# Performance work log

Hardware: AMD Instinct MI355X
Metric: run time of the kernel (lower is better)

## Reference

```python
import jax, jax.numpy as jnp
import numpy as np

B, T, TM, D, H, FF = 4, 1024, 1024, 1024, 16, 4096
HS = D // H
EPS = 1e-5


def _layer_norm(x, g, b):
    m = jnp.mean(x, axis=-1, keepdims=True)
    v = jnp.mean(jnp.square(x - m), axis=-1, keepdims=True)
    return (x - m) / jnp.sqrt(v + EPS) * g + b


def _mha(q_in, k_in, v_in, wq, bq, wk, bk, wv, bv, wo, bo):
    b, t, c = q_in.shape
    tm = k_in.shape[1]
    q = (q_in @ wq + bq).reshape(b, t, H, HS).transpose(0, 2, 1, 3)   # [b,h,t,hs]
    k = (k_in @ wk + bk).reshape(b, tm, H, HS).transpose(0, 2, 1, 3)  # [b,h,tm,hs]
    v = (v_in @ wv + bv).reshape(b, tm, H, HS).transpose(0, 2, 1, 3)
    att = jnp.einsum('bhtd,bhsd->bhts', q, k) * (1.0 / np.sqrt(HS))
    att = jax.nn.softmax(att, axis=-1)                                # [b,h,t,tm]
    y = jnp.einsum('bhts,bhsd->bhtd', att, v)
    y = y.transpose(0, 2, 1, 3).reshape(b, t, c)
    y = y @ wo + bo
    return y, att.mean(axis=1)                                        # attn avg over heads


def setup_inputs() -> dict:
    key = jax.random.key(0)
    ks = jax.random.split(key, 32)
    s = 0.02
    w = lambda k, shape: (jax.random.normal(k, shape, jnp.float32) * s)
    inp = {
        'tgt': jax.random.normal(ks[0], (B, T, D), jnp.float32),
        'memory': jax.random.normal(ks[1], (B, TM, D), jnp.float32),
        # self-attention params
        'sa_wq': w(ks[2], (D, D)), 'sa_bq': jnp.zeros((D,), jnp.float32),
        'sa_wk': w(ks[3], (D, D)), 'sa_bk': jnp.zeros((D,), jnp.float32),
        'sa_wv': w(ks[4], (D, D)), 'sa_bv': jnp.zeros((D,), jnp.float32),
        'sa_wo': w(ks[5], (D, D)), 'sa_bo': jnp.zeros((D,), jnp.float32),
        # cross-attention params
        'ca_wq': w(ks[6], (D, D)), 'ca_bq': jnp.zeros((D,), jnp.float32),
        'ca_wk': w(ks[7], (D, D)), 'ca_bk': jnp.zeros((D,), jnp.float32),
        'ca_wv': w(ks[8], (D, D)), 'ca_bv': jnp.zeros((D,), jnp.float32),
        'ca_wo': w(ks[9], (D, D)), 'ca_bo': jnp.zeros((D,), jnp.float32),
        # FFN
        'w1': w(ks[10], (D, FF)), 'b1': jnp.zeros((FF,), jnp.float32),
        'w2': w(ks[11], (FF, D)), 'b2': jnp.zeros((D,), jnp.float32),
        # LayerNorms
        'ln1_g': jnp.ones((D,), jnp.float32), 'ln1_b': jnp.zeros((D,), jnp.float32),
        'ln2_g': jnp.ones((D,), jnp.float32), 'ln2_b': jnp.zeros((D,), jnp.float32),
        'ln3_g': jnp.ones((D,), jnp.float32), 'ln3_b': jnp.zeros((D,), jnp.float32),
    }
    return inp


def reference(tgt, memory,
              sa_wq, sa_bq, sa_wk, sa_bk, sa_wv, sa_bv, sa_wo, sa_bo,
              ca_wq, ca_bq, ca_wk, ca_bk, ca_wv, ca_bv, ca_wo, ca_bo,
              w1, b1, w2, b2,
              ln1_g, ln1_b, ln2_g, ln2_b, ln3_g, ln3_b):
    x = tgt
    tmp, _ = _mha(x, x, x, sa_wq, sa_bq, sa_wk, sa_bk, sa_wv, sa_bv, sa_wo, sa_bo)
    x = _layer_norm(x + tmp, ln1_g, ln1_b)
    tmp, attention = _mha(x, memory, memory,
                          ca_wq, ca_bq, ca_wk, ca_bk, ca_wv, ca_bv, ca_wo, ca_bo)
    x = _layer_norm(x + tmp, ln2_g, ln2_b)
    tmp = jax.nn.relu(x @ w1 + b1) @ w2 + b2
    x = _layer_norm(x + tmp, ln3_g, ln3_b)
    return x, attention
```

## Files before the change

### kernel.cpp

```cpp
#include <hip/hip_runtime.h>
#include <hip/hip_bf16.h>
#include <cstdint>
#include <cstddef>

using u16 = unsigned short;
typedef __attribute__((ext_vector_type(4))) float f32x4;
typedef __attribute__((ext_vector_type(8))) short bf16x8;
typedef __attribute__((ext_vector_type(4))) short bf16x4;

constexpr int Bc = 4, Tc = 1024, TMc = 1024, Dc = 1024, Hc = 16, HSc = 64, FFc = 4096;
constexpr int BT = Bc * Tc;

__device__ __forceinline__ u16 f2bf(float f) {
  union { float f; uint32_t u; } v; v.f = f;
  uint32_t u = v.u;
  u += 0x7fffu + ((u >> 16) & 1u);
  return (u16)(u >> 16);
}

__device__ __forceinline__ bf16x8 cat8(bf16x4 lo, bf16x4 hi) {
  bf16x8 r;
  r[0] = lo[0]; r[1] = lo[1]; r[2] = lo[2]; r[3] = lo[3];
  r[4] = hi[0]; r[5] = hi[1]; r[6] = hi[2]; r[7] = hi[3];
  return r;
}

__device__ __forceinline__ void gload16(const u16* g, u16* l) {
  __builtin_amdgcn_global_load_lds((const __attribute__((address_space(1))) void*)g,
                                   (__attribute__((address_space(3))) void*)l, 16, 0, 0);
}

__global__ __launch_bounds__(256)
void tconv(const float* __restrict__ in, u16* __restrict__ outp, int K, int N)
{
  __shared__ u16 tile[64][65];
  const int tx = threadIdx.x & 15, ty = threadIdx.x >> 4;
  const int kb = blockIdx.y * 64, nb = blockIdx.x * 64;
  #pragma unroll
  for (int i = 0; i < 4; ++i) {
    const int r = ty + i * 16;
    const float4 v = *(const float4*)(in + (size_t)(kb + r) * N + nb + tx * 4);
    tile[r][tx * 4 + 0] = f2bf(v.x);
    tile[r][tx * 4 + 1] = f2bf(v.y);
    tile[r][tx * 4 + 2] = f2bf(v.z);
    tile[r][tx * 4 + 3] = f2bf(v.w);
  }
  __syncthreads();
  #pragma unroll
  for (int i = 0; i < 4; ++i) {
    const int n = ty + i * 16;
    bf16x4 o;
    o[0] = (short)tile[tx * 4 + 0][n];
    o[1] = (short)tile[tx * 4 + 1][n];
    o[2] = (short)tile[tx * 4 + 2][n];
    o[3] = (short)tile[tx * 4 + 3][n];
    *(bf16x4*)(outp + (size_t)(nb + n) * K + kb + tx * 4) = o;
  }
}

__global__ __launch_bounds__(256)
void cvt_bf16(const float* __restrict__ in, u16* __restrict__ outp, int n4)
{
  const int i = blockIdx.x * 256 + threadIdx.x;
  if (i < n4) {
    const float4 v = ((const float4*)in)[i];
    bf16x4 o;
    o[0] = (short)f2bf(v.x); o[1] = (short)f2bf(v.y);
    o[2] = (short)f2bf(v.z); o[3] = (short)f2bf(v.w);
    ((bf16x4*)outp)[i] = o;
  }
}

template<int MODE, int BMv, int DEPTH>
__global__ __launch_bounds__((BMv == 256) ? 512 : 256)
void gemm_bt(const u16* __restrict__ A, const u16* __restrict__ Bt,
             const float* __restrict__ bias, const float* __restrict__ resid,
             void* __restrict__ outp, int M, int N, int K)
{
  constexpr int BM = BMv, BN = 128, BK = 32;
  constexpr int NTHR = (BM == 256) ? 512 : 256;
  constexpr int RPC = NTHR / 4;
  constexpr int ACALLS = BM / RPC;
  constexpr int BCALLS = BN / RPC;
  constexpr int CALLS = ACALLS + BCALLS;
  constexpr int NB = DEPTH + 1;
  __shared__ __align__(16) u16 As[NB][BM * BK];
  __shared__ __align__(16) u16 Bs[NB][BN * BK];
  const int tid = threadIdx.x;
  const int lane = tid & 63, w = tid >> 6;
  const int wr = w >> 1, wc = w & 1;
  const int hi4 = lane >> 4, lr = lane & 15;

  const int nwg = gridDim.x;
  const int GX = N / BN;
  const int bid0 = (int)blockIdx.x;
  const int L = (bid0 & 7) * (nwg >> 3) + (bid0 >> 3);
  const int bandw = 8 * GX;
  const int band = L / bandw;
  const int rem = L - band * bandw;
  const int m0 = (band * 8 + (rem & 7)) * BM;
  const int n0 = (rem >> 3) * BN;

  const int srow = tid >> 2;
  const int gslot = (tid & 3) ^ ((srow >> 1) & 3);
  const u16* ga = A  + (size_t)(m0 + srow) * K + gslot * 8;
  const u16* gb = Bt + (size_t)(n0 + srow) * K + gslot * 8;
  const int wofs = w * 512;
  const int cswz = (lr >> 1) & 3;

  auto stage = [&](int buf, int kt) {
    #pragma unroll
    for (int j = 0; j < ACALLS; ++j)
      gload16(ga + (size_t)j * RPC * K + kt, &As[buf][j * NTHR * 8 + wofs]);
    #pragma unroll
    for (int j = 0; j < BCALLS; ++j)
      gload16(gb + (size_t)j * RPC * K + kt, &Bs[buf][j * NTHR * 8 + wofs]);
  };

  f32x4 acc[4][4] = {};
  const int nt = K / BK;

  #pragma unroll
  for (int p = 0; p < DEPTH; ++p)
    if (p < nt) stage(p % NB, p * BK);

  int cur = 0;
  for (int t = 0; t < nt; ++t) {
    {
      const int ahead = nt - 1 - t;
      const int cap = (ahead < DEPTH - 1 ? ahead : DEPTH - 1) * CALLS;
      switch (cap) {
        case 0:  asm volatile("s_waitcnt vmcnt(0)"  ::: "memory"); break;
        case 3:  asm volatile("s_waitcnt vmcnt(3)"  ::: "memory"); break;
        case 4:  asm volatile("s_waitcnt vmcnt(4)"  ::: "memory"); break;
        case 8:  asm volatile("s_waitcnt vmcnt(8)"  ::: "memory"); break;
        default: asm volatile("s_waitcnt vmcnt(12)" ::: "memory"); break;
      }
    }
    __builtin_amdgcn_s_barrier();
    __builtin_amdgcn_sched_barrier(0);

    if (t + DEPTH < nt) {
      int b2 = cur + DEPTH; if (b2 >= NB) b2 -= NB;
      stage(b2, (t + DEPTH) * BK);
    }

    bf16x8 af[4], bfr[4];
    #pragma unroll
    for (int mb = 0; mb < 4; ++mb)
      af[mb] = *(const bf16x8*)&As[cur][(wr * 64 + mb * 16 + lr) * BK + (hi4 ^ cswz) * 8];
    #pragma unroll
    for (int nb = 0; nb < 4; ++nb)
      bfr[nb] = *(const bf16x8*)&Bs[cur][(wc * 64 + nb * 16 + lr) * BK + (hi4 ^ cswz) * 8];
    #pragma unroll
    for (int mb = 0; mb < 4; ++mb)
      #pragma unroll
      for (int nb = 0; nb < 4; ++nb)
        acc[mb][nb] = __builtin_amdgcn_mfma_f32_16x16x32_bf16(af[mb], bfr[nb], acc[mb][nb], 0, 0, 0);

    ++cur; if (cur == NB) cur = 0;
  }

  const int orow = m0 + wr * 64 + 4 * hi4;
  const int ocol = n0 + wc * 64 + lr;
  #pragma unroll
  for (int nb = 0; nb < 4; ++nb) {
    const int c = ocol + nb * 16;
    const float bv = bias ? bias[c] : 0.0f;
    #pragma unroll
    for (int mb = 0; mb < 4; ++mb) {
      #pragma unroll
      for (int r = 0; r < 4; ++r) {
        const size_t idx = (size_t)(orow + mb * 16 + r) * N + c;
        float v = acc[mb][nb][r] + bv;
        if (MODE == 1) {
          ((float*)outp)[idx] = v + resid[idx];
        } else {
          if (MODE == 2) v = fmaxf(v, 0.0f);
          ((u16*)outp)[idx] = f2bf(v);
        }
      }
    }
  }
}

__global__ __launch_bounds__(256)
void flash_attn(const u16* __restrict__ Q, const u16* __restrict__ Kb,
                const u16* __restrict__ Vb, u16* __restrict__ Y,
                float* __restrict__ Mout, float* __restrict__ Lout,
                int qstr, int kstr)
{
  constexpr int LDK = 72;
  __shared__ __align__(16) u16 Ks[64 * LDK];
  __shared__ __align__(16) u16 Vt[64 * LDK];
  const int tid = threadIdx.x, lane = tid & 63, w = tid >> 6;
  const int hi4 = lane >> 4, lr = lane & 15;
  const int bh = blockIdx.y, b = bh >> 4, h = bh & 15;
  const int q0 = blockIdx.x * 64 + w * 16;

  bf16x8 qf[2];
  {
    const u16* qp = Q + ((size_t)(b * Tc + q0 + lr)) * qstr + h * HSc;
    #pragma unroll
    for (int ks = 0; ks < 2; ++ks)
      qf[ks] = cat8(*(const bf16x4*)(qp + ks * 32 + 4 * hi4),
                    *(const bf16x4*)(qp + ks * 32 + 16 + 4 * hi4));
  }

  float m_run = -1e30f, l_run = 0.0f;
  f32x4 o[4] = {};

  const int krow = tid >> 3, kcol = (tid & 7) * 8;
  const int vs = tid >> 4, vd = (tid & 15) * 4;

  for (int s0 = 0; s0 < TMc; s0 += 64) {
    const u16* kp = Kb + ((size_t)(b * TMc + s0 + krow)) * kstr + h * HSc + kcol;
    *(bf16x8*)&Ks[krow * LDK + kcol]        = *(const bf16x8*)kp;
    *(bf16x8*)&Ks[(krow + 32) * LDK + kcol] = *(const bf16x8*)(kp + (size_t)32 * kstr);
    #pragma unroll
    for (int rr = 0; rr < 4; ++rr) {
      const int ss = vs + rr * 16;
      bf16x4 vv = *(const bf16x4*)(Vb + ((size_t)(b * TMc + s0 + ss)) * kstr + h * HSc + vd);
      Vt[(vd + 0) * LDK + ss] = (u16)vv[0];
      Vt[(vd + 1) * LDK + ss] = (u16)vv[1];
      Vt[(vd + 2) * LDK + ss] = (u16)vv[2];
      Vt[(vd + 3) * LDK + ss] = (u16)vv[3];
    }
    __syncthreads();

    f32x4 st[4];
    #pragma unroll
    for (int kb2 = 0; kb2 < 4; ++kb2) {
      f32x4 a = {};
      #pragma unroll
      for (int ks = 0; ks < 2; ++ks) {
        const u16* p = &Ks[(kb2 * 16 + lr) * LDK + ks * 32 + 4 * hi4];
        bf16x8 kf = cat8(*(const bf16x4*)p, *(const bf16x4*)(p + 16));
        a = __builtin_amdgcn_mfma_f32_16x16x32_bf16(kf, qf[ks], a, 0, 0, 0);
      }
      st[kb2] = a;
    }

    float cmax = -1e30f;
    #pragma unroll
    for (int kb2 = 0; kb2 < 4; ++kb2)
      #pragma unroll
      for (int r = 0; r < 4; ++r) {
        st[kb2][r] *= 0.125f;
        cmax = fmaxf(cmax, st[kb2][r]);
      }
    cmax = fmaxf(cmax, __shfl_xor(cmax, 16));
    cmax = fmaxf(cmax, __shfl_xor(cmax, 32));
    const float m_new = fmaxf(m_run, cmax);
    const float sc = __expf(m_run - m_new);
    float psum = 0.0f;
    #pragma unroll
    for (int kb2 = 0; kb2 < 4; ++kb2)
      #pragma unroll
      for (int r = 0; r < 4; ++r) {
        const float e = __expf(st[kb2][r] - m_new);
        st[kb2][r] = e;
        psum += e;
      }
    psum += __shfl_xor(psum, 16);
    psum += __shfl_xor(psum, 32);
    l_run = l_run * sc + psum;
    m_run = m_new;

    #pragma unroll
    for (int r = 0; r < 4; ++r) {
      const float osc = __shfl(sc, 4 * hi4 + r);
      #pragma unroll
      for (int nb = 0; nb < 4; ++nb) o[nb][r] *= osc;
    }

    bf16x8 pa[2];
    #pragma unroll
    for (int ks = 0; ks < 2; ++ks) {
      bf16x8 t;
      #pragma unroll
      for (int i = 0; i < 4; ++i) t[i]     = (short)f2bf(st[2 * ks + 0][i]);
      #pragma unroll
      for (int i = 0; i < 4; ++i) t[4 + i] = (short)f2bf(st[2 * ks + 1][i]);
      pa[ks] = t;
    }
    #pragma unroll
    for (int nb = 0; nb < 4; ++nb) {
      #pragma unroll
      for (int ks = 0; ks < 2; ++ks) {
        const u16* p = &Vt[(nb * 16 + lr) * LDK + ks * 32 + 4 * hi4];
        bf16x8 vf = cat8(*(const bf16x4*)p, *(const bf16x4*)(p + 16));
        o[nb] = __builtin_amdgcn_mfma_f32_16x16x32_bf16(pa[ks], vf, o[nb], 0, 0, 0);
      }
    }
    __syncthreads();
  }

  #pragma unroll
  for (int r = 0; r < 4; ++r) {
    const float li = 1.0f / __shfl(l_run, 4 * hi4 + r);
    const size_t yr = ((size_t)(b * Tc + q0 + 4 * hi4 + r)) * Dc + h * HSc;
    #pragma unroll
    for (int nb = 0; nb < 4; ++nb)
      Y[yr + nb * 16 + lr] = f2bf(o[nb][r] * li);
  }
  if (Mout != nullptr && lane < 16) {
    Mout[(size_t)bh * Tc + q0 + lr] = m_run;
    Lout[(size_t)bh * Tc + q0 + lr] = l_run;
  }
}

__global__ __launch_bounds__(256)
void attn_avg(const u16* __restrict__ Q, const u16* __restrict__ Kb,
              const float* __restrict__ Mws, const float* __restrict__ Lws,
              float* __restrict__ outp, int qstr, int kstr)
{
  __shared__ __align__(16) u16 Ks[2][64 * 64];
  __shared__ __align__(16) float avg[64 * 68];
  const int tid = threadIdx.x, lane = tid & 63, w = tid >> 6;
  const int hi4 = lane >> 4, lr = lane & 15;
  const int b = blockIdx.z, qt = blockIdx.y, scn = blockIdx.x;
  const int q0 = qt * 64 + w * 16;
  const int s0 = scn * 64;

  const int srow = w * 8 + (lane >> 3);
  const int scol = ((lane & 7) ^ (lane >> 3)) * 8;
  const u16* kg = Kb + ((size_t)(b * TMc + s0 + srow)) * kstr + scol;
  const size_t skip32 = (size_t)32 * kstr;

  auto stage = [&](int buf, int h) {
    const u16* g = kg + h * HSc;
    gload16(g,          &Ks[buf][w * 512]);
    gload16(g + skip32, &Ks[buf][2048 + w * 512]);
  };

  float acc[4][4] = {};
  const int rsw = lr & 7;

  stage(0, 0);
  #pragma unroll 1
  for (int h = 0; h < Hc; ++h) {
    const int cur = h & 1;
    __syncthreads();
    if (h + 1 < Hc) stage(cur ^ 1, h + 1);

    const u16* qp = Q + ((size_t)(b * Tc + q0 + lr)) * qstr + h * HSc;
    const bf16x8 qf0 = *(const bf16x8*)(qp + 8 * hi4);
    const bf16x8 qf1 = *(const bf16x8*)(qp + 32 + 8 * hi4);
    const float mh = Mws[(size_t)(b * Hc + h) * Tc + q0 + lr];
    const float li = 1.0f / Lws[(size_t)(b * Hc + h) * Tc + q0 + lr];

    #pragma unroll
    for (int kb2 = 0; kb2 < 4; ++kb2) {
      const int row = kb2 * 16 + lr;
      const bf16x8 kf0 = *(const bf16x8*)&Ks[cur][row * 64 + ((hi4     ) ^ rsw) * 8];
      const bf16x8 kf1 = *(const bf16x8*)&Ks[cur][row * 64 + ((hi4 + 4) ^ rsw) * 8];
      f32x4 a = {};
      a = __builtin_amdgcn_mfma_f32_16x16x32_bf16(kf0, qf0, a, 0, 0, 0);
      a = __builtin_amdgcn_mfma_f32_16x16x32_bf16(kf1, qf1, a, 0, 0, 0);
      #pragma unroll
      for (int r = 0; r < 4; ++r)
        acc[kb2][r] += __expf(a[r] * 0.125f - mh) * li;
    }
  }

  __syncthreads();
  #pragma unroll
  for (int kb2 = 0; kb2 < 4; ++kb2)
    #pragma unroll
    for (int r = 0; r < 4; ++r)
      avg[(w * 16 + lr) * 68 + kb2 * 16 + 4 * hi4 + r] = acc[kb2][r] * (1.0f / Hc);
  __syncthreads();
  const int row = tid >> 2, col = (tid & 3) * 16;
  float* gp = outp + ((size_t)(b * Tc + qt * 64 + row)) * TMc + s0 + col;
  #pragma unroll
  for (int j = 0; j < 4; ++j)
    *(f32x4*)(gp + j * 4) = *(const f32x4*)&avg[row * 68 + col + j * 4];
}

__global__ __launch_bounds__(256)
void add_ln(const float* __restrict__ in, const float* __restrict__ g,
            const float* __restrict__ bb, float* __restrict__ outf,
            u16* __restrict__ outb)
{
  __shared__ float red1[4];
  __shared__ float red2[4];
  const int tid = threadIdx.x, lane = tid & 63, w = tid >> 6;
  const size_t row = blockIdx.x;
  float4 v = ((const float4*)(in + row * Dc))[tid];
  float s = v.x + v.y + v.z + v.w;
  #pragma unroll
  for (int o = 32; o >= 1; o >>= 1) s += __shfl_xor(s, o);
  if (lane == 0) red1[w] = s;
  __syncthreads();
  s = red1[0] + red1[1] + red1[2] + red1[3];
  const float mean = s * (1.0f / Dc);
  const float dx = v.x - mean, dy = v.y - mean, dz = v.z - mean, dw = v.w - mean;
  float s2 = dx * dx + dy * dy + dz * dz + dw * dw;
  #pragma unroll
  for (int o = 32; o >= 1; o >>= 1) s2 += __shfl_xor(s2, o);
  if (lane == 0) red2[w] = s2;
  __syncthreads();
  s2 = red2[0] + red2[1] + red2[2] + red2[3];
  const float rstd = rsqrtf(s2 * (1.0f / Dc) + 1e-5f);
  const float4 gv = ((const float4*)g)[tid];
  const float4 bv = ((const float4*)bb)[tid];
  float4 o4;
  o4.x = dx * rstd * gv.x + bv.x;
  o4.y = dy * rstd * gv.y + bv.y;
  o4.z = dz * rstd * gv.z + bv.z;
  o4.w = dw * rstd * gv.w + bv.w;
  ((float4*)(outf + row * Dc))[tid] = o4;
  if (outb != nullptr) {
    bf16x4 ob;
    ob[0] = (short)f2bf(o4.x); ob[1] = (short)f2bf(o4.y);
    ob[2] = (short)f2bf(o4.z); ob[3] = (short)f2bf(o4.w);
    *(bf16x4*)(outb + row * Dc + (size_t)tid * 4) = ob;
  }
}

extern "C" void kernel_launch(void* const* d_in, const int* in_sizes, int n_in,
                              void* d_out, int out_size, void* d_ws, size_t ws_size,
                              hipStream_t stream)
{
  (void)in_sizes; (void)n_in; (void)out_size; (void)ws_size;
  const float* tgt = (const float*)d_in[0];
  const float* mem = (const float*)d_in[1];
  const float* Wf[10]   = { (const float*)d_in[2],  (const float*)d_in[4],  (const float*)d_in[6],  (const float*)d_in[8],
                            (const float*)d_in[10], (const float*)d_in[12], (const float*)d_in[14], (const float*)d_in[16],
                            (const float*)d_in[18], (const float*)d_in[20] };
  const float* bias_[10]= { (const float*)d_in[3],  (const float*)d_in[5],  (const float*)d_in[7],  (const float*)d_in[9],
                            (const float*)d_in[11], (const float*)d_in[13], (const float*)d_in[15], (const float*)d_in[17],
                            (const float*)d_in[19], (const float*)d_in[21] };
  const float* ln1g = (const float*)d_in[22]; const float* ln1b = (const float*)d_in[23];
  const float* ln2g = (const float*)d_in[24]; const float* ln2b = (const float*)d_in[25];
  const float* ln3g = (const float*)d_in[26]; const float* ln3b = (const float*)d_in[27];

  char* wsp = (char*)d_ws;
  auto alloc = [&](size_t bytes) -> char* {
    char* p = wsp;
    wsp += (bytes + 255) & ~(size_t)255;
    return p;
  };
  u16* wT[8];
  for (int i = 0; i < 8; ++i) wT[i] = (u16*)alloc((size_t)Dc * Dc * 2);
  u16* w1T  = (u16*)alloc((size_t)Dc * FFc * 2);
  u16* w2T  = (u16*)alloc((size_t)Dc * FFc * 2);
  u16* xb   = (u16*)alloc((size_t)BT * Dc * 2);
  u16* memb = (u16*)alloc((size_t)BT * Dc * 2);
  u16* qb   = (u16*)alloc((size_t)BT * Dc * 2);
  u16* yb   = (u16*)alloc((size_t)BT * Dc * 2);
  u16* ffb  = (u16*)alloc((size_t)BT * FFc * 2);
  float* res = (float*)alloc((size_t)BT * Dc * 4);
  float* xf  = (float*)alloc((size_t)BT * Dc * 4);
  float* mws = (float*)alloc((size_t)Bc * Hc * Tc * 4);
  float* lws = (float*)alloc((size_t)Bc * Hc * Tc * 4);
  float* bqkv = (float*)alloc(3 * Dc * 4);
  float* bkv  = (float*)alloc(2 * Dc * 4);

  u16* qkv    = ffb;
  u16* kvb    = ffb;
  u16* wqkvT  = (u16*)res;

  float* out_x   = (float*)d_out;
  float* out_att = out_x + (size_t)BT * Dc;

  for (int i = 0; i < 8; ++i)
    tconv<<<dim3(Dc / 64, Dc / 64), 256, 0, stream>>>(Wf[i], wT[i], Dc, Dc);
  tconv<<<dim3(FFc / 64, Dc / 64), 256, 0, stream>>>(Wf[8], w1T, Dc, FFc);
  tconv<<<dim3(Dc / 64, FFc / 64), 256, 0, stream>>>(Wf[9], w2T, FFc, Dc);
  cvt_bf16<<<BT * Dc / 4 / 256, 256, 0, stream>>>(tgt, xb, BT * Dc / 4);
  cvt_bf16<<<BT * Dc / 4 / 256, 256, 0, stream>>>(mem, memb, BT * Dc / 4);

  for (int j = 0; j < 3; ++j) {
    hipMemcpyAsync(wqkvT + (size_t)j * Dc * Dc, wT[j], (size_t)Dc * Dc * 2,
                   hipMemcpyDeviceToDevice, stream);
    hipMemcpyAsync(bqkv + j * Dc, bias_[j], Dc * 4, hipMemcpyDeviceToDevice, stream);
  }
  for (int j = 0; j < 2; ++j)
    hipMemcpyAsync(bkv + j * Dc, bias_[5 + j], Dc * 4, hipMemcpyDeviceToDevice, stream);

  const int nD    = (Dc / 128) * (BT / 128);
  const int nQKVw = (3 * Dc / 128) * (BT / 256);
  const int nKVw  = (2 * Dc / 128) * (BT / 256);
  const int nFw   = (FFc / 128) * (BT / 256);
  const dim3 gAtt(Tc / 64, Bc * Hc);
  const dim3 gAvg(TMc / 64, Tc / 64, Bc);

  gemm_bt<0, 256, 2><<<nQKVw, 512, 0, stream>>>(xb, wqkvT, bqkv, nullptr, qkv, BT, 3 * Dc, Dc);
  flash_attn<<<gAtt, 256, 0, stream>>>(qkv, qkv + Dc, qkv + 2 * Dc, yb,
                                       nullptr, nullptr, 3 * Dc, 3 * Dc);
  gemm_bt<1, 128, 4><<<nD, 256, 0, stream>>>(yb, wT[3], bias_[3], tgt, res, BT, Dc, Dc);
  add_ln<<<BT, 256, 0, stream>>>(res, ln1g, ln1b, xf, xb);

  gemm_bt<0, 128, 4><<<nD, 256, 0, stream>>>(xb, wT[4], bias_[4], nullptr, qb, BT, Dc, Dc);
  gemm_bt<0, 256, 2><<<nKVw, 512, 0, stream>>>(memb, wT[5], bkv, nullptr, kvb, BT, 2 * Dc, Dc);
  flash_attn<<<gAtt, 256, 0, stream>>>(qb, kvb, kvb + Dc, yb, mws, lws, Dc, 2 * Dc);
  attn_avg<<<gAvg, 256, 0, stream>>>(qb, kvb, mws, lws, out_att, Dc, 2 * Dc);
  gemm_bt<1, 128, 4><<<nD, 256, 0, stream>>>(yb, wT[7], bias_[7], xf, res, BT, Dc, Dc);
  add_ln<<<BT, 256, 0, stream>>>(res, ln2g, ln2b, xf, xb);

  gemm_bt<2, 256, 2><<<nFw, 512, 0, stream>>>(xb,  w1T, bias_[8], nullptr, ffb, BT, FFc, Dc);
  gemm_bt<1, 128, 4><<<nD, 256, 0, stream>>>(ffb, w2T, bias_[9], xf, res, BT, Dc, FFc);
  add_ln<<<BT, 256, 0, stream>>>(res, ln3g, ln3b, out_x, nullptr);
}
```

Measured before the change: 535.7 us.

## Split-K the FFN down-projection into four bf16 partials reduced in LayerNorm

```diff
diff --git a/kernel.cpp b/kernel.cpp
--- a/kernel.cpp
+++ b/kernel.cpp
@@ -10,12 +10,17 @@
 
 constexpr int Bc = 4, Tc = 1024, TMc = 1024, Dc = 1024, Hc = 16, HSc = 64, FFc = 4096;
 constexpr int BT = Bc * Tc;
+
+struct Ptr4 { u16* p0; u16* p1; u16* p2; u16* p3; };
 
 __device__ __forceinline__ u16 f2bf(float f) {
   union { float f; uint32_t u; } v; v.f = f;
   uint32_t u = v.u;
   u += 0x7fffu + ((u >> 16) & 1u);
   return (u16)(u >> 16);
+}
+__device__ __forceinline__ float b2f(u16 u) {
+  union { float f; uint32_t u32; } v; v.u32 = (uint32_t)u << 16; return v.f;
 }
 
 __device__ __forceinline__ bf16x8 cat8(bf16x4 lo, bf16x4 hi) {
@@ -75,7 +80,7 @@
 __global__ __launch_bounds__((BMv == 256) ? 512 : 256)
 void gemm_bt(const u16* __restrict__ A, const u16* __restrict__ Bt,
              const float* __restrict__ bias, const float* __restrict__ resid,
-             void* __restrict__ outp, int M, int N, int K)
+             void* __restrict__ outp, int M, int N, int K, int Kch, Ptr4 P)
 {
   constexpr int BM = BMv, BN = 128, BK = 32;
   constexpr int NTHR = (BM == 256) ? 512 : 256;
@@ -101,10 +106,12 @@
   const int m0 = (band * 8 + (rem & 7)) * BM;
   const int n0 = (rem >> 3) * BN;
 
+  const int k0 = (MODE == 3) ? (int)blockIdx.y * Kch : 0;
+
   const int srow = tid >> 2;
   const int gslot = (tid & 3) ^ ((srow >> 1) & 3);
-  const u16* ga = A  + (size_t)(m0 + srow) * K + gslot * 8;
-  const u16* gb = Bt + (size_t)(n0 + srow) * K + gslot * 8;
+  const u16* ga = A  + (size_t)(m0 + srow) * K + k0 + gslot * 8;
+  const u16* gb = Bt + (size_t)(n0 + srow) * K + k0 + gslot * 8;
   const int wofs = w * 512;
   const int cswz = (lr >> 1) & 3;
 
@@ -118,7 +125,7 @@
   };
 
   f32x4 acc[4][4] = {};
-  const int nt = K / BK;
+  const int nt = Kch / BK;
 
   #pragma unroll
   for (int p = 0; p < DEPTH; ++p)
@@ -161,12 +168,18 @@
     ++cur; if (cur == NB) cur = 0;
   }
 
+  u16* pout = nullptr;
+  if (MODE == 3) {
+    const int sk = blockIdx.y;
+    pout = (sk == 0) ? P.p0 : (sk == 1) ? P.p1 : (sk == 2) ? P.p2 : P.p3;
+  }
+
   const int orow = m0 + wr * 64 + 4 * hi4;
   const int ocol = n0 + wc * 64 + lr;
   #pragma unroll
   for (int nb = 0; nb < 4; ++nb) {
     const int c = ocol + nb * 16;
-    const float bv = bias ? bias[c] : 0.0f;
+    const float bv = (MODE != 3 && bias) ? bias[c] : 0.0f;
     #pragma unroll
     for (int mb = 0; mb < 4; ++mb) {
       #pragma unroll
@@ -175,6 +188,8 @@
         float v = acc[mb][nb][r] + bv;
         if (MODE == 1) {
           ((float*)outp)[idx] = v + resid[idx];
+        } else if (MODE == 3) {
+          pout[idx] = f2bf(v);
         } else {
           if (MODE == 2) v = fmaxf(v, 0.0f);
           ((u16*)outp)[idx] = f2bf(v);
@@ -417,6 +432,54 @@
     ob[2] = (short)f2bf(o4.z); ob[3] = (short)f2bf(o4.w);
     *(bf16x4*)(outb + row * Dc + (size_t)tid * 4) = ob;
   }
+}
+
+__global__ __launch_bounds__(256)
+void add_ln4(const u16* __restrict__ p0, const u16* __restrict__ p1,
+             const u16* __restrict__ p2, const u16* __restrict__ p3,
+             const float* __restrict__ bias2, const float* __restrict__ resid,
+             const float* __restrict__ g, const float* __restrict__ bb,
+             float* __restrict__ outf)
+{
+  __shared__ float red1[4];
+  __shared__ float red2[4];
+  const int tid = threadIdx.x, lane = tid & 63, w = tid >> 6;
+  const size_t row = blockIdx.x;
+  const size_t base = row * Dc + (size_t)tid * 4;
+  const bf16x4 a0 = *(const bf16x4*)(p0 + base);
+  const bf16x4 a1 = *(const bf16x4*)(p1 + base);
+  const bf16x4 a2 = *(const bf16x4*)(p2 + base);
+  const bf16x4 a3 = *(const bf16x4*)(p3 + base);
+  const float4 rv = ((const float4*)(resid + row * Dc))[tid];
+  const float4 b2 = ((const float4*)bias2)[tid];
+  float4 v;
+  v.x = b2f((u16)a0[0]) + b2f((u16)a1[0]) + b2f((u16)a2[0]) + b2f((u16)a3[0]) + b2.x + rv.x;
+  v.y = b2f((u16)a0[1]) + b2f((u16)a1[1]) + b2f((u16)a2[1]) + b2f((u16)a3[1]) + b2.y + rv.y;
+  v.z = b2f((u16)a0[2]) + b2f((u16)a1[2]) + b2f((u16)a2[2]) + b2f((u16)a3[2]) + b2.z + rv.z;
+  v.w = b2f((u16)a0[3]) + b2f((u16)a1[3]) + b2f((u16)a2[3]) + b2f((u16)a3[3]) + b2.w + rv.w;
+  float s = v.x + v.y + v.z + v.w;
+  #pragma unroll
+  for (int o = 32; o >= 1; o >>= 1) s += __shfl_xor(s, o);
+  if (lane == 0) red1[w] = s;
+  __syncthreads();
+  s = red1[0] + red1[1] + red1[2] + red1[3];
+  const float mean = s * (1.0f / Dc);
+  const float dx = v.x - mean, dy = v.y - mean, dz = v.z - mean, dw = v.w - mean;
+  float s2 = dx * dx + dy * dy + dz * dz + dw * dw;
+  #pragma unroll
+  for (int o = 32; o >= 1; o >>= 1) s2 += __shfl_xor(s2, o);
+  if (lane == 0) red2[w] = s2;
+  __syncthreads();
+  s2 = red2[0] + red2[1] + red2[2] + red2[3];
+  const float rstd = rsqrtf(s2 * (1.0f / Dc) + 1e-5f);
+  const float4 gv = ((const float4*)g)[tid];
+  const float4 bv = ((const float4*)bb)[tid];
+  float4 o4;
+  o4.x = dx * rstd * gv.x + bv.x;
+  o4.y = dy * rstd * gv.y + bv.y;
+  o4.z = dz * rstd * gv.z + bv.z;
+  o4.w = dw * rstd * gv.w + bv.w;
+  ((float4*)(outf + row * Dc))[tid] = o4;
 }
 
 extern "C" void kernel_launch(void* const* d_in, const int* in_sizes, int n_in,
@@ -461,9 +524,12 @@
   u16* qkv    = ffb;
   u16* kvb    = ffb;
   u16* wqkvT  = (u16*)res;
+  Ptr4 fp { qb, yb, memb, (u16*)res };
 
   float* out_x   = (float*)d_out;
   float* out_att = out_x + (size_t)BT * Dc;
+
+  Ptr4 z { nullptr, nullptr, nullptr, nullptr };
 
   for (int i = 0; i < 8; ++i)
     tconv<<<dim3(Dc / 64, Dc / 64), 256, 0, stream>>>(Wf[i], wT[i], Dc, Dc);
@@ -487,20 +553,22 @@
   const dim3 gAtt(Tc / 64, Bc * Hc);
   const dim3 gAvg(TMc / 64, Tc / 64, Bc);
 
-  gemm_bt<0, 256, 2><<<nQKVw, 512, 0, stream>>>(xb, wqkvT, bqkv, nullptr, qkv, BT, 3 * Dc, Dc);
+  gemm_bt<0, 256, 2><<<nQKVw, 512, 0, stream>>>(xb, wqkvT, bqkv, nullptr, qkv, BT, 3 * Dc, Dc, Dc, z);
   flash_attn<<<gAtt, 256, 0, stream>>>(qkv, qkv + Dc, qkv + 2 * Dc, yb,
                                        nullptr, nullptr, 3 * Dc, 3 * Dc);
-  gemm_bt<1, 128, 4><<<nD, 256, 0, stream>>>(yb, wT[3], bias_[3], tgt, res, BT, Dc, Dc);
+  gemm_bt<1, 128, 2><<<nD, 256, 0, stream>>>(yb, wT[3], bias_[3], tgt, res, BT, Dc, Dc, Dc, z);
   add_ln<<<BT, 256, 0, stream>>>(res, ln1g, ln1b, xf, xb);
 
-  gemm_bt<0, 128, 4><<<nD, 256, 0, stream>>>(xb, wT[4], bias_[4], nullptr, qb, BT, Dc, Dc);
-  gemm_bt<0, 256, 2><<<nKVw, 512, 0, stream>>>(memb, wT[5], bkv, nullptr, kvb, BT, 2 * Dc, Dc);
+  gemm_bt<0, 128, 2><<<nD, 256, 0, stream>>>(xb, wT[4], bias_[4], nullptr, qb, BT, Dc, Dc, Dc, z);
+  gemm_bt<0, 256, 2><<<nKVw, 512, 0, stream>>>(memb, wT[5], bkv, nullptr, kvb, BT, 2 * Dc, Dc, Dc, z);
   flash_attn<<<gAtt, 256, 0, stream>>>(qb, kvb, kvb + Dc, yb, mws, lws, Dc, 2 * Dc);
   attn_avg<<<gAvg, 256, 0, stream>>>(qb, kvb, mws, lws, out_att, Dc, 2 * Dc);
-  gemm_bt<1, 128, 4><<<nD, 256, 0, stream>>>(yb, wT[7], bias_[7], xf, res, BT, Dc, Dc);
+  gemm_bt<1, 128, 2><<<nD, 256, 0, stream>>>(yb, wT[7], bias_[7], xf, res, BT, Dc, Dc, Dc, z);
   add_ln<<<BT, 256, 0, stream>>>(res, ln2g, ln2b, xf, xb);
 
-  gemm_bt<2, 256, 2><<<nFw, 512, 0, stream>>>(xb,  w1T, bias_[8], nullptr, ffb, BT, FFc, Dc);
-  gemm_bt<1, 128, 4><<<nD, 256, 0, stream>>>(ffb, w2T, bias_[9], xf, res, BT, Dc, FFc);
-  add_ln<<<BT, 256, 0, stream>>>(res, ln3g, ln3b, out_x, nullptr);
-}
+  gemm_bt<2, 256, 2><<<nFw, 512, 0, stream>>>(xb,  w1T, bias_[8], nullptr, ffb, BT, FFc, Dc, Dc, z);
+  gemm_bt<3, 128, 2><<<dim3(nD, 4), 256, 0, stream>>>(ffb, w2T, nullptr, nullptr, nullptr,
+                                                      BT, Dc, FFc, FFc / 4, fp);
+  add_ln4<<<BT, 256, 0, stream>>>(fp.p0, fp.p1, fp.p2, fp.p3, bias_[9], xf,
+                                  ln3g, ln3b, out_x);
+}
```

Measured after the change: 507.0 us. 5.4% less time.
